# Kernel tuning notes

Hardware: AMD Instinct MI355X
Metric: run time of the kernel (lower is better)

## Reference

```python
import jax, jax.numpy as jnp
import numpy as np

B, N, T, H = 32, 512, 3, 8
F_IN, F_HID, F_OUT = 768, 64, 64
NEG_SLOPE = 0.2
NEG_INF = -1e9


def setup_inputs() -> dict:
    key = jax.random.key(0)
    ks = jax.random.split(key, 16)
    s = 0.05
    emb = jax.random.normal(ks[0], (B, N, F_IN), jnp.float32)
    adj = jax.random.randint(ks[1], (B, N, N), 0, 2).astype(jnp.int32)
    adj = adj.at[:, jnp.arange(N), jnp.arange(N)].set(1)  # self loops so no empty rows
    vt_idx = jax.random.randint(ks[2], (B, N), 0, T)
    v_types = jax.nn.one_hot(vt_idx, T, dtype=jnp.float32)
    # layer 1 GAT params: per-type weights [T,H,f_in,f_out]
    w1 = jax.random.normal(ks[3], (T, H, F_IN, F_HID), jnp.float32) * s
    a_src1 = jax.random.normal(ks[4], (H, F_HID), jnp.float32) * s
    a_dst1 = jax.random.normal(ks[5], (H, F_HID), jnp.float32) * s
    b1 = jnp.zeros((F_HID,), jnp.float32)
    # layer 2 GAT (single head, f_in = H*F_HID)
    w2 = jax.random.normal(ks[6], (T, 1, H * F_HID, F_OUT), jnp.float32) * s
    a_src2 = jax.random.normal(ks[7], (1, F_OUT), jnp.float32) * s
    a_dst2 = jax.random.normal(ks[8], (1, F_OUT), jnp.float32) * s
    b2 = jnp.zeros((F_OUT,), jnp.float32)
    # MLP classifier: fc1 d->3d, fc2 3d->d, fc3 d->2
    fc1_w = jax.random.normal(ks[9], (F_OUT, 3 * F_OUT), jnp.float32) * s
    fc1_b = jnp.zeros((3 * F_OUT,), jnp.float32)
    fc2_w = jax.random.normal(ks[10], (3 * F_OUT, F_OUT), jnp.float32) * s
    fc2_b = jnp.zeros((F_OUT,), jnp.float32)
    fc3_w = jax.random.normal(ks[11], (F_OUT, 2), jnp.float32) * s
    fc3_b = jnp.zeros((2,), jnp.float32)
    return dict(emb=emb, adj=adj, v_types=v_types,
                w1=w1, a_src1=a_src1, a_dst1=a_dst1, b1=b1,
                w2=w2, a_src2=a_src2, a_dst2=a_dst2, b2=b2,
                fc1_w=fc1_w, fc1_b=fc1_b, fc2_w=fc2_w, fc2_b=fc2_b,
                fc3_w=fc3_w, fc3_b=fc3_b)


def _leaky_relu(x):
    return jnp.where(x >= 0, x, NEG_SLOPE * x)


def _gat(h, adj_mask, vt, w, a_src, a_dst, bias):
    # h: [B,N,f_in], vt: [B,N,T] one-hot, w: [T,Hd,f_in,f_out]
    # per-type projection then select node's type
    hpt = jnp.einsum('bni,thio->bntho', h, w)          # [B,N,T,Hd,f_out]
    hp = jnp.einsum('bnt,bntho->bnho', vt, hpt)        # [B,N,Hd,f_out]
    src = jnp.einsum('bnho,ho->bhn', hp, a_src)        # [B,Hd,N]
    dst = jnp.einsum('bnho,ho->bhn', hp, a_dst)
    e = _leaky_relu(src[:, :, :, None] + dst[:, :, None, :])  # [B,Hd,N,N]
    e = jnp.where(adj_mask[:, None, :, :], e, NEG_INF)
    attn = jax.nn.softmax(e, axis=-1)                  # attn_dropout=0.0 -> identity
    out = jnp.einsum('bhnm,bmho->bhno', attn, hp) + bias
    return out                                         # [B,Hd,N,f_out]


def reference(emb, adj, v_types, w1, a_src1, a_dst1, b1,
              w2, a_src2, a_dst2, b2,
              fc1_w, fc1_b, fc2_w, fc2_b, fc3_w, fc3_b):
    adj_mask = adj > 0
    x = _gat(emb, adj_mask, v_types, w1, a_src1, a_dst1, b1)    # [B,H,N,F_HID]
    x = jnp.transpose(x, (0, 2, 1, 3)).reshape(B, N, H * F_HID)  # concat heads
    x = jax.nn.elu(x)                                            # dropout: eval mode (identity)
    x = _gat(x, adj_mask, v_types, w2, a_src2, a_dst2, b2)       # [B,1,N,F_OUT]
    x = jax.nn.elu(x)
    x = x[:, 0, :, :]                                            # squeeze head dim -> [B,N,F_OUT]
    left = x[:, 0, :]
    right = x[:, 1, :]
    v = left * right
    v = jax.nn.relu(v @ fc1_w + fc1_b)
    v = jax.nn.relu(v @ fc2_w + fc2_b)
    scores = v @ fc3_w + fc3_b
    return jax.nn.log_softmax(scores, axis=1)
```

## Files before the change

kernel.cpp:

```cpp
#include <hip/hip_runtime.h>

#define BB   32
#define NN   512
#define NH   8
#define FIN  768
#define FHID 64
#define NROWS (BB*NN)

typedef __attribute__((ext_vector_type(8))) short bf16x8;
typedef __attribute__((ext_vector_type(4))) short s16x4;
typedef __attribute__((ext_vector_type(4))) float f32x4;
typedef unsigned long long u64;
typedef unsigned short u16;
typedef long i64;

__device__ __forceinline__ float lrelu_f(float s){ return fmaxf(s, 0.2f*s); }
__device__ __forceinline__ float elu_f(float s){ return s > 0.f ? s : expm1f(s); }
__device__ __forceinline__ short f2bf(float f){
  unsigned u = __float_as_uint(f);
  return (short)((u + 0x7fffu + ((u >> 16) & 1u)) >> 16);
}
__device__ __forceinline__ float bf2f(short s){
  return __uint_as_float(((unsigned)(u16)s) << 16);
}
__device__ __forceinline__ unsigned cvt_pk_bf16(float lo, float hi){
  unsigned r;
  asm("v_cvt_pk_bf16_f32 %0, %1, %2" : "=v"(r) : "v"(lo), "v"(hi));
  return r;
}
__device__ __forceinline__ float exp2_fast(float x){
  float r;
  asm("v_exp_f32 %0, %1" : "=v"(r) : "v"(x));
  return r;
}
__device__ __forceinline__ unsigned cvt_pk_fp8(float lo, float hi){
  return (unsigned)__builtin_amdgcn_cvt_pk_fp8_f32(lo, hi, 0, false);
}

__global__ __launch_bounds__(256) void prep_kernel(
    const int* __restrict__ adj,
    u64* __restrict__ maskw)
{
  int row  = blockIdx.x * 4 + (threadIdx.x >> 6);
  int lane = threadIdx.x & 63;
  const int* arow = adj + (long)row * NN;
  #pragma unroll
  for (int w = 0; w < 8; ++w) {
    u64 bal = __ballot(arow[w*64 + lane] > 0);
    if (lane == 0) maskw[(long)row*8 + w] = bal;
  }
}

__global__ __launch_bounds__(256) void rowlist_kernel(
    const float* __restrict__ vt,
    int* __restrict__ rowlist, int* __restrict__ counts)
{
  __shared__ int lc[3];
  __shared__ int lbase[3];
  int tid = threadIdx.x;
  int row = blockIdx.x * 256 + tid;
  if (tid < 3) lc[tid] = 0;
  __syncthreads();
  const float* v = vt + (long)row*3;
  int t = v[1] > 0.5f ? 1 : (v[2] > 0.5f ? 2 : 0);
  int p = atomicAdd(&lc[t], 1);
  __syncthreads();
  if (tid < 3) lbase[tid] = atomicAdd(&counts[tid], lc[tid]);
  __syncthreads();
  rowlist[t*NROWS + lbase[t] + p] = row;
}

__global__ __launch_bounds__(256) void conv_w(
    const float* __restrict__ w1, const float* __restrict__ w2,
    u16* __restrict__ w1t, u16* __restrict__ w2t)
{
  __shared__ float tile[64][68];
  int bid = blockIdx.x, tid = threadIdx.x;
  const float* src; u16* dst; int K;
  if (bid < 24) { src = w1 + (long)bid*768*64; dst = w1t + (long)bid*64*768; K = 768; }
  else { int t = bid - 24; src = w2 + (long)t*512*64; dst = w2t + (long)t*64*512; K = 512; }
  int kq = blockIdx.y;
  int kstart = kq * (K >> 2), kend = kstart + (K >> 2);

  for (int k0 = kstart; k0 < kend; k0 += 64) {
    __syncthreads();
    #pragma unroll
    for (int i = 0; i < 4; ++i) {
      int kk = i*16 + (tid >> 4);
      int oo = (tid & 15) * 4;
      float4 v = *(const float4*)(src + (long)(k0 + kk)*64 + oo);
      *(float4*)&tile[kk][oo] = v;
    }
    __syncthreads();
    int o = tid >> 2, kp = (tid & 3) * 16;
    unsigned pk[8];
    #pragma unroll
    for (int j = 0; j < 8; ++j)
      pk[j] = cvt_pk_bf16(tile[kp + 2*j][o], tile[kp + 2*j + 1][o]);
    u16* d = dst + (long)o*K + k0 + kp;
    #pragma unroll
    for (int j = 0; j < 8; ++j) *(unsigned*)(d + 2*j) = pk[j];
    __syncthreads();
  }
}

#define G1_WRITE(A0,A1,B1,B2,BUFA,BUFB) { \
    unsigned lo0 = cvt_pk_bf16((A0).x, (A0).y), hi0 = cvt_pk_bf16((A0).z, (A0).w); \
    unsigned lo1 = cvt_pk_bf16((A1).x, (A1).y), hi1 = cvt_pk_bf16((A1).z, (A1).w); \
    *(uint2*)&(BUFA)[aw0] = make_uint2(lo0, hi0); \
    *(uint2*)&(BUFA)[aw1] = make_uint2(lo1, hi1); \
    *(bf16x8*)&(BUFB)[bw0] = (B1); \
    *(bf16x8*)&(BUFB)[bw1] = (B2); }

#define G1_COMPUTE(BUFA,BUFB) { \
    bf16x8 af_[2], bf_[4]; \
    _Pragma("unroll") \
    for (int fr = 0; fr < 2; ++fr) \
      af_[fr] = *(const bf16x8*)&(BUFA)[(lg*66 + wr*32 + fr*16 + l15)*8]; \
    _Pragma("unroll") \
    for (int cf = 0; cf < 4; ++cf) \
      bf_[cf] = *(const bf16x8*)&(BUFB)[(lg*130 + wc*64 + cf*16 + l15)*8]; \
    _Pragma("unroll") \
    for (int fr = 0; fr < 2; ++fr) \
      _Pragma("unroll") \
      for (int cf = 0; cf < 4; ++cf) \
        acc[fr][cf] = __builtin_amdgcn_mfma_f32_16x16x32_bf16(af_[fr], bf_[cf], acc[fr][cf], 0, 0, 0); }

__global__ __launch_bounds__(256) void gemm1_mfma(
    const float* __restrict__ emb,
    const u16* __restrict__ w1t,
    const int* __restrict__ rowlist, const int* __restrict__ counts,
    u16* __restrict__ hp1b)
{
  int i   = blockIdx.x;
  int t   = i / 352;
  int r   = i - t*352;
  int cnt = counts[t];
  int xcd = r & 7;
  int q   = r >> 3;
  int hb  = q & 3;
  int rb  = (q >> 2) * 8 + xcd;
  int r0  = rb * 64;
  if (r0 >= cnt) return;

  __shared__ short aT[2][4*66*8];
  __shared__ short bT[2][4*130*8];
  __shared__ int rowsS[64];

  int tid = threadIdx.x;
  if (tid < 64) {
    int rr = r0 + tid;
    rowsS[tid] = (rr < cnt) ? rowlist[t*NROWS + rr] : -1;
  }
  __syncthreads();

  int ar = tid >> 2, ac = tid & 3;
  int sg = rowsS[ar]; if (sg < 0) sg = rowsS[0];
  const float* aP = emb + (long)sg*768;

  int colb = tid >> 2, off = tid & 3;
  const u16* bP1 = w1t + (((long)t*8 + hb*2 + 0)*64 + colb)*768;
  const u16* bP2 = w1t + (((long)t*8 + hb*2 + 1)*64 + colb)*768;

  int wv = tid >> 6, l = tid & 63;
  int wr = wv >> 1, wc = wv & 1;
  int l15 = l & 15, lg = l >> 4;

  int aw0 = (( (ac>>1)     )*66 + ar)*8 + (ac&1)*4;
  int aw1 = (( 2 + (ac>>1) )*66 + ar)*8 + (ac&1)*4;
  int bw0 = (off*130 + colb     )*8;
  int bw1 = (off*130 + colb + 64)*8;

  f32x4 acc[2][4];
  #pragma unroll
  for (int fr = 0; fr < 2; ++fr)
    #pragma unroll
    for (int cf = 0; cf < 4; ++cf) acc[fr][cf] = (f32x4){0.f,0.f,0.f,0.f};

  float4 a0_0 = *(const float4*)(aP + ac*4);
  float4 a1_0 = *(const float4*)(aP + 16 + ac*4);
  bf16x8 b1_0 = *(const bf16x8*)(bP1 + off*8);
  bf16x8 b2_0 = *(const bf16x8*)(bP2 + off*8);
  G1_WRITE(a0_0, a1_0, b1_0, b2_0, aT[0], bT[0]);
  float4 a0_1 = *(const float4*)(aP + 32 + ac*4);
  float4 a1_1 = *(const float4*)(aP + 48 + ac*4);
  bf16x8 b1_1 = *(const bf16x8*)(bP1 + 32 + off*8);
  bf16x8 b2_1 = *(const bf16x8*)(bP2 + 32 + off*8);
  __syncthreads();

  for (int k0 = 0; k0 < 768; k0 += 64) {
    if (k0 + 64 < 768) {
      a0_0 = *(const float4*)(aP + k0 + 64 + ac*4);
      a1_0 = *(const float4*)(aP + k0 + 80 + ac*4);
      b1_0 = *(const bf16x8*)(bP1 + k0 + 64 + off*8);
      b2_0 = *(const bf16x8*)(bP2 + k0 + 64 + off*8);
    }
    G1_COMPUTE(aT[0], bT[0]);
    G1_WRITE(a0_1, a1_1, b1_1, b2_1, aT[1], bT[1]);
    __syncthreads();
    if (k0 + 96 < 768) {
      a0_1 = *(const float4*)(aP + k0 + 96 + ac*4);
      a1_1 = *(const float4*)(aP + k0 + 112 + ac*4);
      b1_1 = *(const bf16x8*)(bP1 + k0 + 96 + off*8);
      b2_1 = *(const bf16x8*)(bP2 + k0 + 96 + off*8);
    }
    G1_COMPUTE(aT[1], bT[1]);
    if (k0 + 64 < 768) {
      G1_WRITE(a0_0, a1_0, b1_0, b2_0, aT[0], bT[0]);
    }
    __syncthreads();
  }

  #pragma unroll
  for (int fr = 0; fr < 2; ++fr) {
    #pragma unroll
    for (int r4 = 0; r4 < 4; ++r4) {
      int rloc = wr*32 + fr*16 + lg*4 + r4;
      int rg = rowsS[rloc];
      if (rg < 0) continue;
      long obase = ((long)(rg >> 9) * 8) * 32768 + (long)(rg & 511) * 64;
      #pragma unroll
      for (int cf = 0; cf < 4; ++cf) {
        int c = wc*64 + cf*16 + l15;
        hp1b[obase + (long)(hb*2 + (c >> 6))*32768 + (c & 63)] = (u16)f2bf(acc[fr][cf][r4]);
      }
    }
  }
}

__global__ __launch_bounds__(256) void gemm2_mfma(
    const u16* __restrict__ xbf,
    const u16* __restrict__ w2t,
    const int* __restrict__ rowlist, const int* __restrict__ counts,
    float* __restrict__ hp2)
{
  int i   = blockIdx.x;
  int t   = i >> 8;
  int cnt = counts[t];
  int r0  = (i & 255) * 64;
  if (r0 >= cnt) return;

  __shared__ short aT[4*66*8];
  __shared__ short bT[4*66*8];
  __shared__ int rowsS[64];

  int tid = threadIdx.x;
  if (tid < 64) {
    int rr = r0 + tid;
    rowsS[tid] = (rr < cnt) ? rowlist[t*NROWS + rr] : -1;
  }
  __syncthreads();

  int ar = tid >> 2, ac = tid & 3;
  int sg = rowsS[ar]; if (sg < 0) sg = rowsS[0];
  long apart = ((long)(sg >> 9) * 8) * 32768 + (long)(sg & 511) * 64;

  int colb = tid >> 2, off = tid & 3;
  const u16* bP = w2t + ((long)t*64 + colb)*512;

  int wv = tid >> 6, l = tid & 63;
  int l15 = l & 15, lg = l >> 4;

  f32x4 acc[4];
  #pragma unroll
  for (int cf = 0; cf < 4; ++cf) acc[cf] = (f32x4){0.f,0.f,0.f,0.f};

  int ka0 = ac*8;
  bf16x8 ra = *(const bf16x8*)(xbf + apart + (long)(ka0 >> 6)*32768 + (ka0 & 63));
  bf16x8 rb = *(const bf16x8*)(bP + off*8);

  for (int k0 = 0; k0 < 512; k0 += 32) {
    __syncthreads();
    *(bf16x8*)&aT[(ac*66 + ar)*8]   = ra;
    *(bf16x8*)&bT[(off*66 + colb)*8] = rb;
    __syncthreads();
    if (k0 + 32 < 512) {
      int kn = k0 + 32 + ac*8;
      ra = *(const bf16x8*)(xbf + apart + (long)(kn >> 6)*32768 + (kn & 63));
      rb = *(const bf16x8*)(bP + k0 + 32 + off*8);
    }
    bf16x8 af, bfr[4];
    af = *(const bf16x8*)&aT[(lg*66 + wv*16 + l15)*8];
    #pragma unroll
    for (int cf = 0; cf < 4; ++cf)
      bfr[cf] = *(const bf16x8*)&bT[(lg*66 + cf*16 + l15)*8];
    #pragma unroll
    for (int cf = 0; cf < 4; ++cf)
      acc[cf] = __builtin_amdgcn_mfma_f32_16x16x32_bf16(af, bfr[cf], acc[cf], 0, 0, 0);
  }

  #pragma unroll
  for (int r4 = 0; r4 < 4; ++r4) {
    int rloc = wv*16 + lg*4 + r4;
    int rg = rowsS[rloc];
    if (rg < 0) continue;
    #pragma unroll
    for (int cf = 0; cf < 4; ++cf)
      hp2[(long)rg*64 + cf*16 + l15] = acc[cf][r4];
  }
}

__global__ __launch_bounds__(1024) void gat1_attn(
    const u16* __restrict__ hp1b, const u64* __restrict__ maskw,
    const float* __restrict__ a_src, const float* __restrict__ a_dst,
    const float* __restrict__ b1, u16* __restrict__ xbf)
{
  extern __shared__ char smc[];
  char*  hpTf = smc;
  char*  pSf  = smc + 33792;
  float* srcS = (float*)(smc + 67584);
  float* dstS = (float*)(smc + 69632);
  float* asS  = (float*)(smc + 71680);
  float* adS  = (float*)(smc + 71936);
  float* rcpS = (float*)(smc + 72192);

  const float LOG2E = 1.4426950408889634f;

  int bid = blockIdx.x;
  int bh = bid >> 1, qh = bid & 1;
  int b = bh >> 3, h = bh & 7;
  int tid = threadIdx.x;

  if (tid < 64) asS[tid] = a_src[h*64 + tid];
  else if (tid < 128) adS[tid - 64] = a_dst[h*64 + (tid - 64)];
  __syncthreads();

  {
    int m = tid >> 1, half = tid & 1;
    int koct = m >> 3, kin = m & 7;
    const u16* hpRow = hp1b + ((long)bh*NN + m)*64 + half*32;
    float ps = 0.f, pd = 0.f;
    #pragma unroll
    for (int qq = 0; qq < 4; ++qq) {
      bf16x8 hv = *(const bf16x8*)(hpRow + qq*8);
      int o0 = half*32 + qq*8;
      #pragma unroll
      for (int j = 0; j < 8; ++j) {
        float f = bf2f(hv[j]);
        ps += f * asS[o0 + j];
        pd += f * adS[o0 + j];
        hpTf[(koct*66 + o0 + j)*8 + kin] = (char)(cvt_pk_fp8(f, f) & 0xffu);
      }
    }
    ps += __shfl_xor(ps, 1);
    pd += __shfl_xor(pd, 1);
    if ((tid & 1) == 0) { srcS[m] = ps * LOG2E; dstS[m] = pd * LOG2E; }
  }
  __syncthreads();

  int wv = tid >> 6, lane = tid & 63;
  int l15 = lane & 15, lg = lane >> 4;
  int cgl = wv >> 2, nt = wv & 3;
  int o_out = nt*16 + l15;
  float bb  = b1[o_out];

  float2 dst2[4];
  #pragma unroll
  for (int jj = 0; jj < 4; ++jj)
    dst2[jj] = *(const float2*)&dstS[jj*128 + 2*lane];
  int wsel = lane >> 5;
  unsigned sh = (unsigned)((2*lane) & 63);
  int pbase = ((lane >> 2)*66)*8 + 2*(lane & 3);

  for (int s = 0; s < 4; ++s) {
    int sup = qh*4 + s;
    #pragma unroll
    for (int rr = 0; rr < 4; ++rr) {
      int rloc = wv*4 + rr;
      int row  = sup*64 + rloc;
      float srcv = srcS[row];
      const u64* mrow = maskw + ((long)(b*NN + row))*8;
      float lsum = 0.f;
      #pragma unroll
      for (int jj = 0; jj < 4; ++jj) {
        u64 w = mrow[jj*2 + wsel];
        unsigned bits = (unsigned)(w >> sh) & 3u;
        float s0 = srcv + dst2[jj].x;
        float s1 = srcv + dst2[jj].y;
        float p0 = (bits & 1u) ? exp2_fast(lrelu_f(s0)) : 0.f;
        float p1 = (bits & 2u) ? exp2_fast(lrelu_f(s1)) : 0.f;
        lsum += p0 + p1;
        *(u16*)&pSf[(jj*16*66)*8 + pbase + rloc*8] = (u16)cvt_pk_fp8(p0, p1);
      }
      #pragma unroll
      for (int mk = 1; mk <= 32; mk <<= 1) lsum += __shfl_xor(lsum, mk);
      if (lane == 0) rcpS[rloc] = 1.f / lsum;
    }
    __syncthreads();

    f32x4 acc = {0.f, 0.f, 0.f, 0.f};
    #pragma unroll
    for (int ks = 0; ks < 16; ++ks) {
      int koct = ks*4 + lg;
      i64 af = *(const i64*)&pSf [(koct*66 + cgl*16 + l15)*8];
      i64 bf = *(const i64*)&hpTf[(koct*66 + nt*16  + l15)*8];
      acc = __builtin_amdgcn_mfma_f32_16x16x32_fp8_fp8(af, bf, acc, 0, 0, 0);
    }
    #pragma unroll
    for (int reg = 0; reg < 4; ++reg) {
      int rloc = cgl*16 + lg*4 + reg;
      int row  = sup*64 + rloc;
      float v = elu_f(acc[reg] * rcpS[rloc] + bb);
      xbf[((long)bh*NN + row)*64 + o_out] = (u16)f2bf(v);
    }
    __syncthreads();
  }
}

__global__ __launch_bounds__(256) void gat2_final(
    const float* __restrict__ hp2, const u64* __restrict__ maskw,
    const float* __restrict__ a_src2, const float* __restrict__ a_dst2,
    const float* __restrict__ b2,
    const float* __restrict__ fc1_w, const float* __restrict__ fc1_b,
    const float* __restrict__ fc2_w, const float* __restrict__ fc2_b,
    const float* __restrict__ fc3_w, const float* __restrict__ fc3_b,
    float* __restrict__ out)
{
  extern __shared__ float sm[];
  float* hpS  = sm;
  float* dstS = hpS + 32768;
  float* srcS = dstS + 512;
  float* pS   = srcS + 512;
  float* redS = pS + 512;
  float* outS = redS + 256;
  float* vS   = outS + 128;
  float* y1S  = vS + 64;
  float* redM = y1S + 192;
  float4* hpS4 = (float4*)hpS;

  int b = blockIdx.x;
  int tid = threadIdx.x;
  int og = tid & 15, m16 = tid >> 4;

  for (int it = 0; it < 32; ++it) {
    int fi = it*256 + tid;
    int m = fi >> 4, o4 = fi & 15;
    hpS4[m*16 + o4] = *(const float4*)(hp2 + (long)(b*NN + m)*64 + o4*4);
  }
  __syncthreads();

  float4 as4 = *(const float4*)(a_src2 + og*4);
  float4 ad4 = *(const float4*)(a_dst2 + og*4);
  for (int it = 0; it < 32; ++it) {
    int m = it*16 + m16;
    float4 hv = hpS4[m*16 + og];
    float ls = hv.x*as4.x + hv.y*as4.y + hv.z*as4.z + hv.w*as4.w;
    float ld = hv.x*ad4.x + hv.y*ad4.y + hv.z*ad4.z + hv.w*ad4.w;
    #pragma unroll
    for (int mk = 1; mk <= 8; mk <<= 1) {
      ls += __shfl_xor(ls, mk);
      ld += __shfl_xor(ld, mk);
    }
    if (og == 0) { srcS[m] = ls; dstS[m] = ld; }
  }
  __syncthreads();

  for (int n = 0; n < 2; ++n) {
    float srcv = srcS[n];
    const u64* mrow = maskw + (long)(b*NN + n)*8;
    int m0 = tid, m1 = tid + 256;
    u64 w0 = mrow[m0 >> 6], w1 = mrow[m1 >> 6];
    float s0 = srcv + dstS[m0], s1 = srcv + dstS[m1];
    float e0 = ((w0 >> (m0 & 63)) & 1ull) ? lrelu_f(s0) : -1.0e9f;
    float e1 = ((w1 >> (m1 & 63)) & 1ull) ? lrelu_f(s1) : -1.0e9f;
    float emax = fmaxf(e0, e1);
    #pragma unroll
    for (int mk = 1; mk <= 32; mk <<= 1) emax = fmaxf(emax, __shfl_xor(emax, mk));
    if ((tid & 63) == 0) redM[tid >> 6] = emax;
    __syncthreads();
    emax = fmaxf(fmaxf(redM[0], redM[1]), fmaxf(redM[2], redM[3]));
    float p0 = __expf(e0 - emax), p1 = __expf(e1 - emax);
    pS[m0] = p0; pS[m1] = p1;
    float lsum = p0 + p1;
    #pragma unroll
    for (int mk = 1; mk <= 32; mk <<= 1) lsum += __shfl_xor(lsum, mk);
    if ((tid & 63) == 0) redM[4 + (tid >> 6)] = lsum;
    __syncthreads();
    float rcp = 1.f / (redM[4] + redM[5] + redM[6] + redM[7]);

    float4 acc = make_float4(0.f,0.f,0.f,0.f);
    for (int mm = 0; mm < 32; ++mm) {
      int m = mm*16 + m16;
      float4 hv = hpS4[m*16 + og];
      float p = pS[m];
      acc.x += hv.x*p; acc.y += hv.y*p; acc.z += hv.z*p; acc.w += hv.w*p;
    }
    acc.x += __shfl_xor(acc.x, 16); acc.y += __shfl_xor(acc.y, 16);
    acc.z += __shfl_xor(acc.z, 16); acc.w += __shfl_xor(acc.w, 16);
    acc.x += __shfl_xor(acc.x, 32); acc.y += __shfl_xor(acc.y, 32);
    acc.z += __shfl_xor(acc.z, 32); acc.w += __shfl_xor(acc.w, 32);
    __syncthreads();
    if ((tid & 63) < 16) ((float4*)redS)[(tid >> 6)*16 + (tid & 15)] = acc;
    __syncthreads();
    if (tid < 16) {
      float4 s = make_float4(0.f,0.f,0.f,0.f);
      #pragma unroll
      for (int w = 0; w < 4; ++w) {
        float4 v = ((float4*)redS)[w*16 + tid];
        s.x += v.x; s.y += v.y; s.z += v.z; s.w += v.w;
      }
      float4 bv = *(const float4*)(b2 + tid*4);
      outS[n*64 + tid*4 + 0] = elu_f(s.x*rcp + bv.x);
      outS[n*64 + tid*4 + 1] = elu_f(s.y*rcp + bv.y);
      outS[n*64 + tid*4 + 2] = elu_f(s.z*rcp + bv.z);
      outS[n*64 + tid*4 + 3] = elu_f(s.w*rcp + bv.w);
    }
    __syncthreads();
  }

  if (tid < 64) vS[tid] = outS[tid] * outS[64 + tid];
  __syncthreads();
  if (tid < 192) {
    float a = fc1_b[tid];
    for (int o = 0; o < 64; ++o) a += vS[o]*fc1_w[o*192 + tid];
    y1S[tid] = a > 0.f ? a : 0.f;
  }
  __syncthreads();
  if (tid < 64) {
    float a = fc2_b[tid];
    for (int j = 0; j < 192; ++j) a += y1S[j]*fc2_w[j*64 + tid];
    vS[tid] = a > 0.f ? a : 0.f;
  }
  __syncthreads();
  if (tid == 0) {
    float t0 = fc3_b[0], t1 = fc3_b[1];
    for (int k = 0; k < 64; ++k) {
      float y = vS[k];
      t0 += y*fc3_w[k*2 + 0];
      t1 += y*fc3_w[k*2 + 1];
    }
    float mx = fmaxf(t0, t1);
    float lse = mx + logf(__expf(t0 - mx) + __expf(t1 - mx));
    out[b*2 + 0] = t0 - lse;
    out[b*2 + 1] = t1 - lse;
  }
}

extern "C" void kernel_launch(void* const* d_in, const int* in_sizes, int n_in,
                              void* d_out, int out_size, void* d_ws, size_t ws_size,
                              hipStream_t stream) {
  const float* emb    = (const float*)d_in[0];
  const int*   adj    = (const int*)d_in[1];
  const float* vt     = (const float*)d_in[2];
  const float* w1     = (const float*)d_in[3];
  const float* a_src1 = (const float*)d_in[4];
  const float* a_dst1 = (const float*)d_in[5];
  const float* b1     = (const float*)d_in[6];
  const float* w2     = (const float*)d_in[7];
  const float* a_src2 = (const float*)d_in[8];
  const float* a_dst2 = (const float*)d_in[9];
  const float* b2     = (const float*)d_in[10];
  const float* fc1_w  = (const float*)d_in[11];
  const float* fc1_b  = (const float*)d_in[12];
  const float* fc2_w  = (const float*)d_in[13];
  const float* fc2_b  = (const float*)d_in[14];
  const float* fc3_w  = (const float*)d_in[15];
  const float* fc3_b  = (const float*)d_in[16];

  char* ws = (char*)d_ws;
  int* counts  = (int*)ws;
  int* rowlist = (int*)(ws + 4096);
  u64* maskw   = (u64*)(ws + 204800);
  u16* w1t     = (u16*)(ws + 1310720);
  u16* w2t     = (u16*)(ws + 3670016);
  u16* hp1b    = (u16*)(ws + 3932160);
  float* hp2   = (float*)(ws + 20709376);
  u16* xbf     = (u16*)(ws + 24903680);

  hipMemsetAsync(counts, 0, 16, stream);
  prep_kernel<<<NROWS/4, 256, 0, stream>>>(adj, maskw);
  rowlist_kernel<<<NROWS/256, 256, 0, stream>>>(vt, rowlist, counts);
  conv_w<<<dim3(27, 4), 256, 0, stream>>>(w1, w2, w1t, w2t);

  gemm1_mfma<<<dim3(1056), 256, 0, stream>>>(emb, w1t, rowlist, counts, hp1b);

  size_t sm1 = 72448;
  gat1_attn<<<BB*NH*2, 1024, sm1, stream>>>(hp1b, maskw, a_src1, a_dst1, b1, xbf);

  gemm2_mfma<<<dim3(768), 256, 0, stream>>>(xbf, w2t, rowlist, counts, hp2);

  size_t sm2 = (size_t)(32768 + 512 + 512 + 512 + 256 + 128 + 64 + 192 + 8) * 4;
  gat2_final<<<BB, 256, sm2, stream>>>(hp2, maskw, a_src2, a_dst2, b2,
                                       fc1_w, fc1_b, fc2_w, fc2_b, fc3_w, fc3_b,
                                       (float*)d_out);
}
```

Baseline: 147.0 us.

## Retile W1 into per-k-step tiles and stream B via global_load_lds

Adds a retile kernel that lays out the bf16 W1 weights as contiguous 4096-element tiles per (type, head-pair, k-step). The GEMM1 kernel then loads B tiles straight into LDS with async global_load_lds, bypassing registers. The k-loop drops from a 64-wide step to a 32-wide double-buffered step, with A still converted from fp32 through registers. This trades an extra small kernel launch and workspace reuse (aliasing the hp2 buffer) for fewer VGPR round-trips and fully contiguous B loads. The B LDS tile also loses its padding, which may cause bank conflicts.

```diff
diff --git a/kernel.cpp b/kernel.cpp
--- a/kernel.cpp
+++ b/kernel.cpp
@@ -35,6 +35,11 @@
 }
 __device__ __forceinline__ unsigned cvt_pk_fp8(float lo, float hi){
   return (unsigned)__builtin_amdgcn_cvt_pk_fp8_f32(lo, hi, 0, false);
+}
+__device__ __forceinline__ void gll16(const void* g, void* l){
+  __builtin_amdgcn_global_load_lds(
+      (const __attribute__((address_space(1))) void*)g,
+      (__attribute__((address_space(3))) void*)l, 16, 0, 0);
 }
 
 __global__ __launch_bounds__(256) void prep_kernel(
@@ -104,31 +109,28 @@
   }
 }
 
-#define G1_WRITE(A0,A1,B1,B2,BUFA,BUFB) { \
-    unsigned lo0 = cvt_pk_bf16((A0).x, (A0).y), hi0 = cvt_pk_bf16((A0).z, (A0).w); \
-    unsigned lo1 = cvt_pk_bf16((A1).x, (A1).y), hi1 = cvt_pk_bf16((A1).z, (A1).w); \
-    *(uint2*)&(BUFA)[aw0] = make_uint2(lo0, hi0); \
-    *(uint2*)&(BUFA)[aw1] = make_uint2(lo1, hi1); \
-    *(bf16x8*)&(BUFB)[bw0] = (B1); \
-    *(bf16x8*)&(BUFB)[bw1] = (B2); }
-
-#define G1_COMPUTE(BUFA,BUFB) { \
-    bf16x8 af_[2], bf_[4]; \
-    _Pragma("unroll") \
-    for (int fr = 0; fr < 2; ++fr) \
-      af_[fr] = *(const bf16x8*)&(BUFA)[(lg*66 + wr*32 + fr*16 + l15)*8]; \
-    _Pragma("unroll") \
-    for (int cf = 0; cf < 4; ++cf) \
-      bf_[cf] = *(const bf16x8*)&(BUFB)[(lg*130 + wc*64 + cf*16 + l15)*8]; \
-    _Pragma("unroll") \
-    for (int fr = 0; fr < 2; ++fr) \
-      _Pragma("unroll") \
-      for (int cf = 0; cf < 4; ++cf) \
-        acc[fr][cf] = __builtin_amdgcn_mfma_f32_16x16x32_bf16(af_[fr], bf_[cf], acc[fr][cf], 0, 0, 0); }
+__global__ __launch_bounds__(256) void retile_w1(
+    const u16* __restrict__ w1t, u16* __restrict__ w1tt)
+{
+  int thb = blockIdx.x;
+  int kiter = blockIdx.y;
+  int t = thb >> 2, hb = thb & 3;
+  int tid = threadIdx.x;
+  u16* dst = w1tt + ((long)thb*24 + kiter)*4096;
+  #pragma unroll
+  for (int c = 0; c < 2; ++c) {
+    int u = c*256 + tid;
+    int kg = u >> 7, col = u & 127;
+    int head = hb*2 + (col >> 6), o = col & 63;
+    int k = kiter*32 + kg*8;
+    const u16* s = w1t + (((long)t*8 + head)*64 + o)*768 + k;
+    *(bf16x8*)(dst + u*8) = *(const bf16x8*)s;
+  }
+}
 
 __global__ __launch_bounds__(256) void gemm1_mfma(
     const float* __restrict__ emb,
-    const u16* __restrict__ w1t,
+    const u16* __restrict__ w1tt,
     const int* __restrict__ rowlist, const int* __restrict__ counts,
     u16* __restrict__ hp1b)
 {
@@ -144,7 +146,7 @@
   if (r0 >= cnt) return;
 
   __shared__ short aT[2][4*66*8];
-  __shared__ short bT[2][4*130*8];
+  __shared__ short bT[2][4096];
   __shared__ int rowsS[64];
 
   int tid = threadIdx.x;
@@ -158,9 +160,7 @@
   int sg = rowsS[ar]; if (sg < 0) sg = rowsS[0];
   const float* aP = emb + (long)sg*768;
 
-  int colb = tid >> 2, off = tid & 3;
-  const u16* bP1 = w1t + (((long)t*8 + hb*2 + 0)*64 + colb)*768;
-  const u16* bP2 = w1t + (((long)t*8 + hb*2 + 1)*64 + colb)*768;
+  const u16* bBase = w1tt + ((long)(t*4 + hb)*24)*4096;
 
   int wv = tid >> 6, l = tid & 63;
   int wr = wv >> 1, wc = wv & 1;
@@ -168,8 +168,6 @@
 
   int aw0 = (( (ac>>1)     )*66 + ar)*8 + (ac&1)*4;
   int aw1 = (( 2 + (ac>>1) )*66 + ar)*8 + (ac&1)*4;
-  int bw0 = (off*130 + colb     )*8;
-  int bw1 = (off*130 + colb + 64)*8;
 
   f32x4 acc[2][4];
   #pragma unroll
@@ -177,38 +175,51 @@
     #pragma unroll
     for (int cf = 0; cf < 4; ++cf) acc[fr][cf] = (f32x4){0.f,0.f,0.f,0.f};
 
-  float4 a0_0 = *(const float4*)(aP + ac*4);
-  float4 a1_0 = *(const float4*)(aP + 16 + ac*4);
-  bf16x8 b1_0 = *(const bf16x8*)(bP1 + off*8);
-  bf16x8 b2_0 = *(const bf16x8*)(bP2 + off*8);
-  G1_WRITE(a0_0, a1_0, b1_0, b2_0, aT[0], bT[0]);
-  float4 a0_1 = *(const float4*)(aP + 32 + ac*4);
-  float4 a1_1 = *(const float4*)(aP + 48 + ac*4);
-  bf16x8 b1_1 = *(const bf16x8*)(bP1 + 32 + off*8);
-  bf16x8 b2_1 = *(const bf16x8*)(bP2 + 32 + off*8);
-  __syncthreads();
-
-  for (int k0 = 0; k0 < 768; k0 += 64) {
-    if (k0 + 64 < 768) {
-      a0_0 = *(const float4*)(aP + k0 + 64 + ac*4);
-      a1_0 = *(const float4*)(aP + k0 + 80 + ac*4);
-      b1_0 = *(const bf16x8*)(bP1 + k0 + 64 + off*8);
-      b2_0 = *(const bf16x8*)(bP2 + k0 + 64 + off*8);
-    }
-    G1_COMPUTE(aT[0], bT[0]);
-    G1_WRITE(a0_1, a1_1, b1_1, b2_1, aT[1], bT[1]);
-    __syncthreads();
-    if (k0 + 96 < 768) {
-      a0_1 = *(const float4*)(aP + k0 + 96 + ac*4);
-      a1_1 = *(const float4*)(aP + k0 + 112 + ac*4);
-      b1_1 = *(const bf16x8*)(bP1 + k0 + 96 + off*8);
-      b2_1 = *(const bf16x8*)(bP2 + k0 + 96 + off*8);
-    }
-    G1_COMPUTE(aT[1], bT[1]);
-    if (k0 + 64 < 768) {
-      G1_WRITE(a0_0, a1_0, b1_0, b2_0, aT[0], bT[0]);
-    }
-    __syncthreads();
+  gll16(bBase + tid*8,        &bT[0][tid*8]);
+  gll16(bBase + (256+tid)*8,  &bT[0][(256+tid)*8]);
+  float4 rA0 = *(const float4*)(aP + ac*4);
+  float4 rA1 = *(const float4*)(aP + 16 + ac*4);
+  {
+    unsigned lo0 = cvt_pk_bf16(rA0.x, rA0.y), hi0 = cvt_pk_bf16(rA0.z, rA0.w);
+    unsigned lo1 = cvt_pk_bf16(rA1.x, rA1.y), hi1 = cvt_pk_bf16(rA1.z, rA1.w);
+    *(uint2*)&aT[0][aw0] = make_uint2(lo0, hi0);
+    *(uint2*)&aT[0][aw1] = make_uint2(lo1, hi1);
+  }
+  rA0 = *(const float4*)(aP + 32 + ac*4);
+  rA1 = *(const float4*)(aP + 48 + ac*4);
+  __syncthreads();
+
+  int cur = 0;
+  for (int kiter = 0; kiter < 24; ++kiter) {
+    if (kiter < 23) {
+      const u16* bsrc = bBase + (long)(kiter+1)*4096;
+      gll16(bsrc + tid*8,       &bT[cur^1][tid*8]);
+      gll16(bsrc + (256+tid)*8, &bT[cur^1][(256+tid)*8]);
+    }
+    bf16x8 af_[2], bf_[4];
+    #pragma unroll
+    for (int fr = 0; fr < 2; ++fr)
+      af_[fr] = *(const bf16x8*)&aT[cur][(lg*66 + wr*32 + fr*16 + l15)*8];
+    #pragma unroll
+    for (int cf = 0; cf < 4; ++cf)
+      bf_[cf] = *(const bf16x8*)&bT[cur][(lg*128 + wc*64 + cf*16 + l15)*8];
+    #pragma unroll
+    for (int fr = 0; fr < 2; ++fr)
+      #pragma unroll
+      for (int cf = 0; cf < 4; ++cf)
+        acc[fr][cf] = __builtin_amdgcn_mfma_f32_16x16x32_bf16(af_[fr], bf_[cf], acc[fr][cf], 0, 0, 0);
+    if (kiter < 23) {
+      unsigned lo0 = cvt_pk_bf16(rA0.x, rA0.y), hi0 = cvt_pk_bf16(rA0.z, rA0.w);
+      unsigned lo1 = cvt_pk_bf16(rA1.x, rA1.y), hi1 = cvt_pk_bf16(rA1.z, rA1.w);
+      *(uint2*)&aT[cur^1][aw0] = make_uint2(lo0, hi0);
+      *(uint2*)&aT[cur^1][aw1] = make_uint2(lo1, hi1);
+      if (kiter < 22) {
+        rA0 = *(const float4*)(aP + (kiter+2)*32 + ac*4);
+        rA1 = *(const float4*)(aP + (kiter+2)*32 + 16 + ac*4);
+      }
+    }
+    __syncthreads();
+    cur ^= 1;
   }
 
   #pragma unroll
@@ -565,14 +576,16 @@
   u16* w2t     = (u16*)(ws + 3670016);
   u16* hp1b    = (u16*)(ws + 3932160);
   float* hp2   = (float*)(ws + 20709376);
+  u16* w1tt    = (u16*)(ws + 20709376);
   u16* xbf     = (u16*)(ws + 24903680);
 
   hipMemsetAsync(counts, 0, 16, stream);
   prep_kernel<<<NROWS/4, 256, 0, stream>>>(adj, maskw);
   rowlist_kernel<<<NROWS/256, 256, 0, stream>>>(vt, rowlist, counts);
   conv_w<<<dim3(27, 4), 256, 0, stream>>>(w1, w2, w1t, w2t);
-
-  gemm1_mfma<<<dim3(1056), 256, 0, stream>>>(emb, w1t, rowlist, counts, hp1b);
+  retile_w1<<<dim3(12, 24), 256, 0, stream>>>(w1t, w1tt);
+
+  gemm1_mfma<<<dim3(1056), 256, 0, stream>>>(emb, w1tt, rowlist, counts, hp1b);
 
   size_t sm1 = 72448;
   gat1_attn<<<BB*NH*2, 1024, sm1, stream>>>(hp1b, maskw, a_src1, a_dst1, b1, xbf);
```

New measurement: 143.3 us. -2.5%, faster.
